# Optimization experiments

Hardware: AMD Instinct MI355X
Metric: run time of the kernel (lower is better)

Reference implementation:

```python
import jax, jax.numpy as jnp
import numpy as np

EPS = 1e-5

def _ln(x, g, b):
    mu = jnp.mean(x, axis=-1, keepdims=True)
    var = jnp.mean((x - mu) ** 2, axis=-1, keepdims=True)
    return (x - mu) * jax.lax.rsqrt(var + EPS) * g + b

def setup_inputs() -> dict:
    key = jax.random.key(0)
    B, V, I, H = 32, 48, 24, 768
    ks = jax.random.split(key, 10)
    s = 0.02
    return {
        'variables': jax.random.normal(ks[0], (B, V, H), jnp.float32),
        'interventions': jax.random.normal(ks[1], (B, I, H), jnp.float32),
        # variable_encoder: Linear(H,H) + LayerNorm(H)
        'W_enc': jax.random.normal(ks[2], (H, H), jnp.float32) * s,
        'b_enc': jnp.zeros((H,), jnp.float32),
        'g_enc': jnp.ones((H,), jnp.float32),
        'be_enc': jnp.zeros((H,), jnp.float32),
        # graph_generator: Linear(2H,H) + LN(H) + ReLU + Linear(H,1) + Sigmoid
        'Wg1': jax.random.normal(ks[3], (2 * H, H), jnp.float32) * s,
        'bg1': jnp.zeros((H,), jnp.float32),
        'g_g': jnp.ones((H,), jnp.float32),
        'b_g': jnp.zeros((H,), jnp.float32),
        'Wg2': jax.random.normal(ks[4], (H, 1), jnp.float32) * s,
        'bg2': jnp.zeros((1,), jnp.float32),
        # intervention_predictor: Linear(2H,H) + LN(H) + ReLU + Linear(H,H)
        'Wi1': jax.random.normal(ks[5], (2 * H, H), jnp.float32) * s,
        'bi1': jnp.zeros((H,), jnp.float32),
        'g_i': jnp.ones((H,), jnp.float32),
        'b_i': jnp.zeros((H,), jnp.float32),
        'Wi2': jax.random.normal(ks[6], (H, H), jnp.float32) * s,
        'bi2': jnp.zeros((H,), jnp.float32),
    }

def reference(variables, interventions, W_enc, b_enc, g_enc, be_enc,
              Wg1, bg1, g_g, b_g, Wg2, bg2, Wi1, bi1, g_i, b_i, Wi2, bi2):
    H = variables.shape[-1]
    V = variables.shape[1]
    # variable encoder: Linear + LayerNorm + ReLU
    enc = jax.nn.relu(_ln(variables @ W_enc + b_enc, g_enc, be_enc))  # [B,V,H]

    # graph generator over all ordered pairs (i,j): concat([enc_i, enc_j]) @ Wg1
    # split Wg1 so the concat-matmul becomes two small GEMMs + broadcast add
    hi = jnp.einsum('bvh,hk->bvk', enc, Wg1[:H])   # contribution of enc_i
    hj = jnp.einsum('bvh,hk->bvk', enc, Wg1[H:])   # contribution of enc_j
    h = jax.nn.relu(_ln(hi[:, :, None, :] + hj[:, None, :, :] + bg1, g_g, b_g))  # [B,V,V,H]
    score = jax.nn.sigmoid(jnp.squeeze(h @ Wg2, -1) + bg2[0])  # [B,V,V]
    # diagonal (i==j) is never written in the original -> stays zero
    causal_graph = score * (1.0 - jnp.eye(V, dtype=score.dtype))

    # intervention predictor: concat([intervention_i, enc_j]) -> MLP
    ha = jnp.einsum('bih,hk->bik', interventions, Wi1[:H])  # [B,I,H]
    hb = jnp.einsum('bvh,hk->bvk', enc, Wi1[H:])            # [B,V,H]
    h2 = jax.nn.relu(_ln(ha[:, :, None, :] + hb[:, None, :, :] + bi1, g_i, b_i))  # [B,I,V,H]
    effects = h2 @ Wi2 + bi2  # [B,I,V,H]

    return (effects, causal_graph, enc)
```

## Files before the change

kernel.cpp:

```cpp
#include <hip/hip_runtime.h>
#include <math.h>

#define Bp 32
#define Vp 48
#define Ip 24
#define Hp 768
#define EPS 1e-5f

#define EFFECTS_SIZE (Bp*Ip*Vp*Hp)
#define GRAPH_SIZE   (Bp*Vp*Vp)
#define ENC_SIZE     (Bp*Vp*Hp)
#define INT_SIZE     (Bp*Ip*Hp)
#define MS           (Hp*Hp)

typedef __attribute__((ext_vector_type(8))) short short8;
typedef __attribute__((ext_vector_type(4))) float floatx4;
typedef __attribute__((ext_vector_type(4))) unsigned int uintx4;

__device__ __forceinline__ unsigned short f2bf(float f) {
    unsigned int u = __float_as_uint(f);
    u += 0x7fffu + ((u >> 16) & 1u);
    return (unsigned short)(u >> 16);
}
__device__ __forceinline__ unsigned int f2bf2(float a, float b) {
    return (unsigned int)f2bf(a) | ((unsigned int)f2bf(b) << 16);
}

__global__ __launch_bounds__(256) void pack_weights(
    const float* __restrict__ W_enc, const float* __restrict__ Wg1,
    const float* __restrict__ Wi1, const float* __restrict__ Wi2,
    unsigned short* __restrict__ packed)
{
    const int bid = blockIdx.x;
    const int m = bid / 48;
    const int T = bid - m * 48;
    const float* src;
    switch (m) {
        case 0: src = W_enc; break;
        case 1: src = Wg1; break;
        case 2: src = Wg1 + Hp * Hp; break;
        case 3: src = Wi1 + Hp * Hp; break;
        case 4: src = Wi1; break;
        default: src = Wi2; break;
    }
    unsigned short* dst = packed + (size_t)m * MS;
    const int lane = threadIdx.x & 63;
    const int kq = threadIdx.x >> 6;
    const int col = T * 16 + (lane & 15);
    const int krow0 = (lane >> 4) * 8;
#pragma unroll
    for (int u = 0; u < 6; ++u) {
        const int kb = kq + 4 * u;
        unsigned int w[4];
#pragma unroll
        for (int p2 = 0; p2 < 4; ++p2) {
            float f0 = src[(size_t)(kb * 32 + krow0 + 2 * p2)     * Hp + col];
            float f1 = src[(size_t)(kb * 32 + krow0 + 2 * p2 + 1) * Hp + col];
            w[p2] = f2bf2(f0, f1);
        }
        uintx4 v; v.x = w[0]; v.y = w[1]; v.z = w[2]; v.w = w[3];
        *(uintx4*)(dst + ((size_t)(T * 24 + kb) * 64 + lane) * 8) = v;
    }
}

__global__ __launch_bounds__(256) void convert_inputs(
    const float* __restrict__ vars, const float* __restrict__ intv,
    const float* __restrict__ bg1, const float* __restrict__ bi1,
    unsigned short* __restrict__ varb, unsigned short* __restrict__ intvb,
    float* __restrict__ bias2304)
{
    const int p = blockIdx.x * 256 + threadIdx.x;
    const int VPn = ENC_SIZE / 2;
    if (p < VPn) {
        float2 f = ((const float2*)vars)[p];
        ((unsigned int*)varb)[p] = f2bf2(f.x, f.y);
    } else {
        int q = p - VPn;
        float2 f = ((const float2*)intv)[q];
        ((unsigned int*)intvb)[q] = f2bf2(f.x, f.y);
    }
    if (blockIdx.x == 0) {
        for (int t = threadIdx.x; t < 2304; t += 256)
            bias2304[t] = (t < 768) ? 0.0f : (t < 1536 ? bg1[t - 768] : bi1[t - 1536]);
    }
}

__global__ __launch_bounds__(256) void gemm_mfma(
    const unsigned short* __restrict__ A, const unsigned short* __restrict__ Bpk,
    const float* __restrict__ bias, float* __restrict__ C, int ldc)
{
    __shared__ unsigned short Asl[32 * 776];
    const int tid = threadIdx.x;
    const int wave = tid >> 6, lane = tid & 63;
    const int m0 = blockIdx.x * 32;
    const int n0 = blockIdx.y * 128;

#pragma unroll
    for (int u = 0; u < 12; ++u) {
        const int chunk = tid + 256 * u;
        const int r = chunk / 96, c = chunk - r * 96;
        uintx4 v = *(const uintx4*)(A + (size_t)(m0 + r) * Hp + c * 8);
        *(uintx4*)(&Asl[r * 776 + c * 8]) = v;
    }
    __syncthreads();

    const int mrow = lane & 15, kq = lane >> 4;
    const floatx4 z = {0.f, 0.f, 0.f, 0.f};
    floatx4 acc00 = z, acc01 = z, acc10 = z, acc11 = z;
    const int Tg0 = (n0 >> 4) + wave * 2;
    const unsigned short* Bb0 = Bpk + ((size_t)(Tg0 * 24) * 64 + lane) * 8;
    const unsigned short* Bb1 = Bpk + ((size_t)((Tg0 + 1) * 24) * 64 + lane) * 8;

#pragma unroll
    for (int kb = 0; kb < 24; ++kb) {
        short8 a0 = *(const short8*)&Asl[mrow * 776 + kb * 32 + kq * 8];
        short8 a1 = *(const short8*)&Asl[(16 + mrow) * 776 + kb * 32 + kq * 8];
        short8 b0 = *(const short8*)(Bb0 + (size_t)kb * 512);
        short8 b1 = *(const short8*)(Bb1 + (size_t)kb * 512);
        acc00 = __builtin_amdgcn_mfma_f32_16x16x32_bf16(a0, b0, acc00, 0, 0, 0);
        acc01 = __builtin_amdgcn_mfma_f32_16x16x32_bf16(a0, b1, acc01, 0, 0, 0);
        acc10 = __builtin_amdgcn_mfma_f32_16x16x32_bf16(a1, b0, acc10, 0, 0, 0);
        acc11 = __builtin_amdgcn_mfma_f32_16x16x32_bf16(a1, b1, acc11, 0, 0, 0);
    }

    floatx4 acc[2][2] = {{acc00, acc01}, {acc10, acc11}};
#pragma unroll
    for (int nt = 0; nt < 2; ++nt) {
        const int colg = n0 + wave * 32 + nt * 16 + mrow;
        const float bv = bias ? bias[colg] : 0.0f;
#pragma unroll
        for (int mt = 0; mt < 2; ++mt) {
#pragma unroll
            for (int r = 0; r < 4; ++r) {
                const int row = m0 + mt * 16 + kq * 4 + r;
                C[(size_t)row * ldc + colg] = acc[mt][nt][r] + bv;
            }
        }
    }
}

__global__ __launch_bounds__(256) void ln_relu(
    const float* __restrict__ pre, const float* __restrict__ g,
    const float* __restrict__ be, float* __restrict__ encf,
    unsigned short* __restrict__ encb)
{
    const int wave = threadIdx.x >> 6, lane = threadIdx.x & 63;
    const int row = blockIdx.x * 4 + wave;
    const float2* rp = (const float2*)(pre + (size_t)row * Hp);
    float2 x[6]; float s = 0.f, q = 0.f;
#pragma unroll
    for (int c = 0; c < 6; ++c) {
        x[c] = rp[lane + 64 * c];
        s += x[c].x + x[c].y;
        q += x[c].x * x[c].x + x[c].y * x[c].y;
    }
#pragma unroll
    for (int m = 1; m < 64; m <<= 1) { s += __shfl_xor(s, m, 64); q += __shfl_xor(q, m, 64); }
    const float mu = s * (1.0f / Hp);
    const float var = q * (1.0f / Hp) - mu * mu;
    const float rs = rsqrtf(var + EPS);
    float2* of = (float2*)(encf + (size_t)row * Hp);
    unsigned int* ob = (unsigned int*)(encb + (size_t)row * Hp);
#pragma unroll
    for (int c = 0; c < 6; ++c) {
        const float2 g2 = ((const float2*)g)[lane + 64 * c];
        const float2 b2 = ((const float2*)be)[lane + 64 * c];
        float y0 = fmaxf((x[c].x - mu) * rs * g2.x + b2.x, 0.f);
        float y1 = fmaxf((x[c].y - mu) * rs * g2.y + b2.y, 0.f);
        of[lane + 64 * c] = make_float2(y0, y1);
        ob[lane + 64 * c] = f2bf2(y0, y1);
    }
}

__global__ __launch_bounds__(256) void graph_kernel(
    const float* __restrict__ ws2, const float* __restrict__ gg_,
    const float* __restrict__ bb_, const float* __restrict__ Wg2,
    const float* __restrict__ bg2, float* __restrict__ out)
{
    const int wave = threadIdx.x >> 6, lane = threadIdx.x & 63;
    const int p = blockIdx.x;
    const int b = p / Vp, i = p - b * Vp;
    const float* hi_row = ws2 + (size_t)p * 2304;
    float ri[12], gg[12], bb[12], w2[12];
#pragma unroll
    for (int c = 0; c < 12; ++c) {
        const int k = lane + 64 * c;
        ri[c] = hi_row[k]; gg[c] = gg_[k]; bb[c] = bb_[k]; w2[c] = Wg2[k];
    }
    const float bg2v = bg2[0];
    const int j0 = wave * 12;
    for (int jj = 0; jj < 12; ++jj) {
        const int j = j0 + jj;
        const float* hj_row = ws2 + (size_t)(b * Vp + j) * 2304 + 768;
        float x[12], s = 0.f, q = 0.f;
#pragma unroll
        for (int c = 0; c < 12; ++c) {
            x[c] = ri[c] + hj_row[lane + 64 * c];
            s += x[c]; q += x[c] * x[c];
        }
#pragma unroll
        for (int m = 1; m < 64; m <<= 1) { s += __shfl_xor(s, m, 64); q += __shfl_xor(q, m, 64); }
        const float mu = s * (1.0f / Hp);
        const float var = q * (1.0f / Hp) - mu * mu;
        const float rs = rsqrtf(var + EPS);
        float pd = 0.f;
#pragma unroll
        for (int c = 0; c < 12; ++c) {
            float y = fmaxf((x[c] - mu) * rs * gg[c] + bb[c], 0.f);
            pd = fmaf(y, w2[c], pd);
        }
#pragma unroll
        for (int m = 1; m < 64; m <<= 1) pd += __shfl_xor(pd, m, 64);
        if (lane == 0) {
            float sc = (i == j) ? 0.0f : 1.0f / (1.0f + expf(-(pd + bg2v)));
            out[(size_t)p * Vp + j] = sc;
        }
    }
}

__global__ __launch_bounds__(256) void effects_mfma(
    const float* __restrict__ ha, const float* __restrict__ ws2,
    const float* __restrict__ g_i, const float* __restrict__ b_i,
    const unsigned short* __restrict__ Bpk, const float* __restrict__ bi2,
    float* __restrict__ out)
{
    __shared__ unsigned short Asl[32 * 776];
    const int tid = threadIdx.x, wave = tid >> 6, lane = tid & 63;
    const int m0 = blockIdx.x * 32;

    float2 gv[6], bv[6];
#pragma unroll
    for (int c = 0; c < 6; ++c) {
        gv[c] = ((const float2*)g_i)[lane + 64 * c];
        bv[c] = ((const float2*)b_i)[lane + 64 * c];
    }

#pragma unroll
    for (int u = 0; u < 8; ++u) {
        const int lr = wave * 8 + u;
        const int r = m0 + lr;
        const int bi = r / 48, j = r - bi * 48;
        const int b = bi / Ip;
        const float2* hap = (const float2*)(ha + (size_t)bi * Hp);
        const float2* hbp = (const float2*)(ws2 + (size_t)(b * Vp + j) * 2304 + 1536);
        float2 x[6]; float s = 0.f, q = 0.f;
#pragma unroll
        for (int c = 0; c < 6; ++c) {
            float2 a2 = hap[lane + 64 * c];
            float2 h2 = hbp[lane + 64 * c];
            x[c].x = a2.x + h2.x; x[c].y = a2.y + h2.y;
            s += x[c].x + x[c].y;
            q += x[c].x * x[c].x + x[c].y * x[c].y;
        }
#pragma unroll
        for (int m = 1; m < 64; m <<= 1) { s += __shfl_xor(s, m, 64); q += __shfl_xor(q, m, 64); }
        const float mu = s * (1.0f / Hp);
        const float var = q * (1.0f / Hp) - mu * mu;
        const float rs = rsqrtf(var + EPS);
#pragma unroll
        for (int c = 0; c < 6; ++c) {
            float y0 = fmaxf((x[c].x - mu) * rs * gv[c].x + bv[c].x, 0.f);
            float y1 = fmaxf((x[c].y - mu) * rs * gv[c].y + bv[c].y, 0.f);
            *(unsigned int*)(&Asl[lr * 776 + (lane + 64 * c) * 2]) = f2bf2(y0, y1);
        }
    }
    __syncthreads();

    const int mrow = lane & 15, kq = lane >> 4;
    const floatx4 z = {0.f, 0.f, 0.f, 0.f};
#pragma unroll
    for (int G = 0; G < 4; ++G) {
        const int Tg = wave * 12 + G * 3;
        floatx4 acc[2][3];
#pragma unroll
        for (int mt = 0; mt < 2; ++mt)
#pragma unroll
            for (int nt = 0; nt < 3; ++nt) acc[mt][nt] = z;
        const unsigned short* Bb0 = Bpk + ((size_t)((Tg + 0) * 24) * 64 + lane) * 8;
        const unsigned short* Bb1 = Bpk + ((size_t)((Tg + 1) * 24) * 64 + lane) * 8;
        const unsigned short* Bb2 = Bpk + ((size_t)((Tg + 2) * 24) * 64 + lane) * 8;
#pragma unroll
        for (int kb = 0; kb < 24; ++kb) {
            short8 a0 = *(const short8*)&Asl[mrow * 776 + kb * 32 + kq * 8];
            short8 a1 = *(const short8*)&Asl[(16 + mrow) * 776 + kb * 32 + kq * 8];
            short8 b0 = *(const short8*)(Bb0 + (size_t)kb * 512);
            short8 b1 = *(const short8*)(Bb1 + (size_t)kb * 512);
            short8 b2 = *(const short8*)(Bb2 + (size_t)kb * 512);
            acc[0][0] = __builtin_amdgcn_mfma_f32_16x16x32_bf16(a0, b0, acc[0][0], 0, 0, 0);
            acc[1][0] = __builtin_amdgcn_mfma_f32_16x16x32_bf16(a1, b0, acc[1][0], 0, 0, 0);
            acc[0][1] = __builtin_amdgcn_mfma_f32_16x16x32_bf16(a0, b1, acc[0][1], 0, 0, 0);
            acc[1][1] = __builtin_amdgcn_mfma_f32_16x16x32_bf16(a1, b1, acc[1][1], 0, 0, 0);
            acc[0][2] = __builtin_amdgcn_mfma_f32_16x16x32_bf16(a0, b2, acc[0][2], 0, 0, 0);
            acc[1][2] = __builtin_amdgcn_mfma_f32_16x16x32_bf16(a1, b2, acc[1][2], 0, 0, 0);
        }
#pragma unroll
        for (int nt = 0; nt < 3; ++nt) {
            const int colg = (Tg + nt) * 16 + mrow;
            const float biasv = bi2[colg];
#pragma unroll
            for (int mt = 0; mt < 2; ++mt) {
#pragma unroll
                for (int r = 0; r < 4; ++r) {
                    const int row = m0 + mt * 16 + kq * 4 + r;
                    out[(size_t)row * Hp + colg] = acc[mt][nt][r] + biasv;
                }
            }
        }
    }
}

extern "C" void kernel_launch(void* const* d_in, const int* in_sizes, int n_in,
                              void* d_out, int out_size, void* d_ws, size_t ws_size,
                              hipStream_t stream) {
    const float* variables     = (const float*)d_in[0];
    const float* interventions = (const float*)d_in[1];
    const float* W_enc  = (const float*)d_in[2];
    const float* b_enc  = (const float*)d_in[3];
    const float* g_enc  = (const float*)d_in[4];
    const float* be_enc = (const float*)d_in[5];
    const float* Wg1 = (const float*)d_in[6];
    const float* bg1 = (const float*)d_in[7];
    const float* g_g = (const float*)d_in[8];
    const float* b_g = (const float*)d_in[9];
    const float* Wg2 = (const float*)d_in[10];
    const float* bg2 = (const float*)d_in[11];
    const float* Wi1 = (const float*)d_in[12];
    const float* bi1 = (const float*)d_in[13];
    const float* g_i = (const float*)d_in[14];
    const float* b_i = (const float*)d_in[15];
    const float* Wi2 = (const float*)d_in[16];
    const float* bi2 = (const float*)d_in[17];

    float* out = (float*)d_out;
    float* effects = out;
    float* graph = out + EFFECTS_SIZE;
    float* enc_f = out + EFFECTS_SIZE + GRAPH_SIZE;

    char* wsb = (char*)d_ws;
    unsigned short* packedW = (unsigned short*)wsb;
    float* ws2  = (float*)(wsb + 7077888);
    float* pre1 = ws2;
    float* ha   = (float*)(wsb + 7077888 + 14155776);
    unsigned short* varb  = (unsigned short*)(wsb + 23592960);
    unsigned short* intvb = (unsigned short*)(wsb + 25952256);
    unsigned short* encb  = (unsigned short*)(wsb + 27131904);
    float* bias2304 = (float*)(wsb + 29491200);

    pack_weights<<<288, 256, 0, stream>>>(W_enc, Wg1, Wi1, Wi2, packedW);
    convert_inputs<<<3456, 256, 0, stream>>>(variables, interventions, bg1, bi1,
                                             varb, intvb, bias2304);
    gemm_mfma<<<dim3(48, 6), 256, 0, stream>>>(varb, packedW, b_enc, pre1, Hp);
    ln_relu<<<384, 256, 0, stream>>>(pre1, g_enc, be_enc, enc_f, encb);
    gemm_mfma<<<dim3(48, 18), 256, 0, stream>>>(encb, packedW + (size_t)1 * MS,
                                                bias2304, ws2, 2304);
    gemm_mfma<<<dim3(24, 6), 256, 0, stream>>>(intvb, packedW + (size_t)4 * MS,
                                               nullptr, ha, Hp);
    graph_kernel<<<Bp * Vp, 256, 0, stream>>>(ws2, g_g, b_g, Wg2, bg2, graph);
    effects_mfma<<<(Bp * Ip * Vp) / 32, 256, 0, stream>>>(ha, ws2, g_i, b_i,
                                                          packedW + (size_t)5 * MS,
                                                          bi2, effects);
}
```

Measured before the change: 329.7 us.

## Retile GEMMs to 48-row blocks with swizzled LDS and register prefetch

The GEMM and effects kernels now use 48-row blocks (one b,i pair per effects block), each wave computing a 3x6 grid of 16x16 MFMA tiles. A is stored in LDS in MFMA fragment order with an XOR swizzle, and B and A fragments are prefetched into rotating register buffers across k-steps. The aim is more operand reuse per load and better latency hiding, and the weight packing kernel is split into more blocks for parallelism. The costs are much higher register pressure and far fewer blocks for the small GEMMs (32 or 16), which could leave many CUs idle.

```diff
diff --git a/kernel.cpp b/kernel.cpp
--- a/kernel.cpp
+++ b/kernel.cpp
@@ -10,7 +10,6 @@
 #define EFFECTS_SIZE (Bp*Ip*Vp*Hp)
 #define GRAPH_SIZE   (Bp*Vp*Vp)
 #define ENC_SIZE     (Bp*Vp*Hp)
-#define INT_SIZE     (Bp*Ip*Hp)
 #define MS           (Hp*Hp)
 
 typedef __attribute__((ext_vector_type(8))) short short8;
@@ -32,8 +31,10 @@
     unsigned short* __restrict__ packed)
 {
     const int bid = blockIdx.x;
-    const int m = bid / 48;
-    const int T = bid - m * 48;
+    const int m = bid / 288;
+    const int rem = bid - m * 288;
+    const int T = rem / 6;
+    const int u = rem - T * 6;
     const float* src;
     switch (m) {
         case 0: src = W_enc; break;
@@ -48,19 +49,16 @@
     const int kq = threadIdx.x >> 6;
     const int col = T * 16 + (lane & 15);
     const int krow0 = (lane >> 4) * 8;
-#pragma unroll
-    for (int u = 0; u < 6; ++u) {
-        const int kb = kq + 4 * u;
-        unsigned int w[4];
-#pragma unroll
-        for (int p2 = 0; p2 < 4; ++p2) {
-            float f0 = src[(size_t)(kb * 32 + krow0 + 2 * p2)     * Hp + col];
-            float f1 = src[(size_t)(kb * 32 + krow0 + 2 * p2 + 1) * Hp + col];
-            w[p2] = f2bf2(f0, f1);
-        }
-        uintx4 v; v.x = w[0]; v.y = w[1]; v.z = w[2]; v.w = w[3];
-        *(uintx4*)(dst + ((size_t)(T * 24 + kb) * 64 + lane) * 8) = v;
-    }
+    const int kb = kq + 4 * u;
+    unsigned int w[4];
+#pragma unroll
+    for (int p2 = 0; p2 < 4; ++p2) {
+        float f0 = src[(size_t)(kb * 32 + krow0 + 2 * p2)     * Hp + col];
+        float f1 = src[(size_t)(kb * 32 + krow0 + 2 * p2 + 1) * Hp + col];
+        w[p2] = f2bf2(f0, f1);
+    }
+    uintx4 v; v.x = w[0]; v.y = w[1]; v.z = w[2]; v.w = w[3];
+    *(uintx4*)(dst + ((size_t)(T * 24 + kb) * 64 + lane) * 8) = v;
 }
 
 __global__ __launch_bounds__(256) void convert_inputs(
@@ -85,56 +83,82 @@
     }
 }
 
-__global__ __launch_bounds__(256) void gemm_mfma(
+__global__ __launch_bounds__(256) void gemm48(
     const unsigned short* __restrict__ A, const unsigned short* __restrict__ Bpk,
     const float* __restrict__ bias, float* __restrict__ C, int ldc)
 {
-    __shared__ unsigned short Asl[32 * 776];
-    const int tid = threadIdx.x;
-    const int wave = tid >> 6, lane = tid & 63;
-    const int m0 = blockIdx.x * 32;
-    const int n0 = blockIdx.y * 128;
-
-#pragma unroll
-    for (int u = 0; u < 12; ++u) {
-        const int chunk = tid + 256 * u;
-        const int r = chunk / 96, c = chunk - r * 96;
-        uintx4 v = *(const uintx4*)(A + (size_t)(m0 + r) * Hp + c * 8);
-        *(uintx4*)(&Asl[r * 776 + c * 8]) = v;
+    __shared__ unsigned short Asl[3 * 24 * 64 * 8];
+    const int tid = threadIdx.x, wave = tid >> 6, lane = tid & 63;
+    const int m0 = blockIdx.x * 48;
+
+#pragma unroll
+    for (int uu = 0; uu < 18; ++uu) {
+        const int s = tid + 256 * uu;
+        const int mt = s / 1536;
+        const int r2 = s - mt * 1536;
+        const int kb = r2 >> 6;
+        const int L  = r2 & 63;
+        const int mrow = L & 15, kq = L >> 4;
+        uintx4 v = *(const uintx4*)(A + (size_t)(m0 + mt * 16 + mrow) * Hp + kb * 32 + kq * 8);
+        const int phys = (mt * 24 + kb) * 64 + (L ^ (kb & 7));
+        *(uintx4*)(&Asl[phys * 8]) = v;
     }
     __syncthreads();
 
     const int mrow = lane & 15, kq = lane >> 4;
     const floatx4 z = {0.f, 0.f, 0.f, 0.f};
-    floatx4 acc00 = z, acc01 = z, acc10 = z, acc11 = z;
-    const int Tg0 = (n0 >> 4) + wave * 2;
-    const unsigned short* Bb0 = Bpk + ((size_t)(Tg0 * 24) * 64 + lane) * 8;
-    const unsigned short* Bb1 = Bpk + ((size_t)((Tg0 + 1) * 24) * 64 + lane) * 8;
-
-#pragma unroll
-    for (int kb = 0; kb < 24; ++kb) {
-        short8 a0 = *(const short8*)&Asl[mrow * 776 + kb * 32 + kq * 8];
-        short8 a1 = *(const short8*)&Asl[(16 + mrow) * 776 + kb * 32 + kq * 8];
-        short8 b0 = *(const short8*)(Bb0 + (size_t)kb * 512);
-        short8 b1 = *(const short8*)(Bb1 + (size_t)kb * 512);
-        acc00 = __builtin_amdgcn_mfma_f32_16x16x32_bf16(a0, b0, acc00, 0, 0, 0);
-        acc01 = __builtin_amdgcn_mfma_f32_16x16x32_bf16(a0, b1, acc01, 0, 0, 0);
-        acc10 = __builtin_amdgcn_mfma_f32_16x16x32_bf16(a1, b0, acc10, 0, 0, 0);
-        acc11 = __builtin_amdgcn_mfma_f32_16x16x32_bf16(a1, b1, acc11, 0, 0, 0);
-    }
-
-    floatx4 acc[2][2] = {{acc00, acc01}, {acc10, acc11}};
-#pragma unroll
-    for (int nt = 0; nt < 2; ++nt) {
-        const int colg = n0 + wave * 32 + nt * 16 + mrow;
-        const float bv = bias ? bias[colg] : 0.0f;
-#pragma unroll
-        for (int mt = 0; mt < 2; ++mt) {
-#pragma unroll
-            for (int r = 0; r < 4; ++r) {
-                const int row = m0 + mt * 16 + kq * 4 + r;
-                C[(size_t)row * ldc + colg] = acc[mt][nt][r] + bv;
+
+#pragma unroll
+    for (int G = 0; G < 2; ++G) {
+        const int Tg0 = blockIdx.y * 48 + wave * 12 + G * 6;
+        const unsigned short* Bbase = Bpk + (size_t)Tg0 * 12288 + lane * 8;
+        floatx4 acc[3][6];
+#pragma unroll
+        for (int mt = 0; mt < 3; ++mt)
+#pragma unroll
+            for (int nt = 0; nt < 6; ++nt) acc[mt][nt] = z;
+
+        short8 bbuf[3][6], abuf[2][3];
+#pragma unroll
+        for (int nt = 0; nt < 6; ++nt) {
+            bbuf[0][nt] = *(const short8*)(Bbase + (size_t)nt * 12288);
+            bbuf[1][nt] = *(const short8*)(Bbase + (size_t)nt * 12288 + 512);
+        }
+#pragma unroll
+        for (int mt = 0; mt < 3; ++mt)
+            abuf[0][mt] = *(const short8*)(&Asl[((mt * 24) * 64 + lane) * 8]);
+
+#pragma unroll
+        for (int kb = 0; kb < 24; ++kb) {
+            if (kb + 2 < 24) {
+#pragma unroll
+                for (int nt = 0; nt < 6; ++nt)
+                    bbuf[(kb + 2) % 3][nt] =
+                        *(const short8*)(Bbase + (size_t)nt * 12288 + (kb + 2) * 512);
             }
+            if (kb + 1 < 24) {
+#pragma unroll
+                for (int mt = 0; mt < 3; ++mt)
+                    abuf[(kb + 1) & 1][mt] = *(const short8*)(
+                        &Asl[((mt * 24 + kb + 1) * 64 + (lane ^ ((kb + 1) & 7))) * 8]);
+            }
+#pragma unroll
+            for (int mt = 0; mt < 3; ++mt)
+#pragma unroll
+                for (int nt = 0; nt < 6; ++nt)
+                    acc[mt][nt] = __builtin_amdgcn_mfma_f32_16x16x32_bf16(
+                        abuf[kb & 1][mt], bbuf[kb % 3][nt], acc[mt][nt], 0, 0, 0);
+        }
+
+#pragma unroll
+        for (int nt = 0; nt < 6; ++nt) {
+            const int colg = (Tg0 + nt) * 16 + mrow;
+            const float bv = bias ? bias[colg] : 0.0f;
+#pragma unroll
+            for (int mt = 0; mt < 3; ++mt)
+#pragma unroll
+                for (int r = 0; r < 4; ++r)
+                    C[(size_t)(m0 + mt * 16 + kq * 4 + r) * ldc + colg] = acc[mt][nt][r] + bv;
         }
     }
 }
@@ -218,50 +242,67 @@
     }
 }
 
-__global__ __launch_bounds__(256) void effects_mfma(
+__global__ __launch_bounds__(256) void effects48(
     const float* __restrict__ ha, const float* __restrict__ ws2,
     const float* __restrict__ g_i, const float* __restrict__ b_i,
     const unsigned short* __restrict__ Bpk, const float* __restrict__ bi2,
     float* __restrict__ out)
 {
-    __shared__ unsigned short Asl[32 * 776];
+    __shared__ unsigned short Asl[3 * 24 * 64 * 8];
     const int tid = threadIdx.x, wave = tid >> 6, lane = tid & 63;
-    const int m0 = blockIdx.x * 32;
-
-    float2 gv[6], bv[6];
-#pragma unroll
-    for (int c = 0; c < 6; ++c) {
-        gv[c] = ((const float2*)g_i)[lane + 64 * c];
-        bv[c] = ((const float2*)b_i)[lane + 64 * c];
-    }
-
-#pragma unroll
-    for (int u = 0; u < 8; ++u) {
-        const int lr = wave * 8 + u;
-        const int r = m0 + lr;
-        const int bi = r / 48, j = r - bi * 48;
-        const int b = bi / Ip;
-        const float2* hap = (const float2*)(ha + (size_t)bi * Hp);
-        const float2* hbp = (const float2*)(ws2 + (size_t)(b * Vp + j) * 2304 + 1536);
-        float2 x[6]; float s = 0.f, q = 0.f;
+    const int bi = blockIdx.x;
+    const int b = bi / Ip;
+    const int half = lane >> 5, hl = lane & 31;
+
+    const floatx4* hap = (const floatx4*)(ha + (size_t)bi * Hp);
+    const floatx4* gp = (const floatx4*)g_i;
+    const floatx4* bp = (const floatx4*)b_i;
+    floatx4 hav[6], gv[6], bv[6];
+#pragma unroll
+    for (int t = 0; t < 3; ++t) {
+        hav[2*t]   = hap[2*hl + 64*t];     hav[2*t+1] = hap[2*hl + 1 + 64*t];
+        gv[2*t]    = gp[2*hl + 64*t];      gv[2*t+1]  = gp[2*hl + 1 + 64*t];
+        bv[2*t]    = bp[2*hl + 64*t];      bv[2*t+1]  = bp[2*hl + 1 + 64*t];
+    }
+
+#pragma unroll
+    for (int p = 0; p < 6; ++p) {
+        const int u = wave * 12 + 2 * p + half;
+        const floatx4* hbp = (const floatx4*)(ws2 + (size_t)(b * Vp + u) * 2304 + 1536);
+        floatx4 x[6]; float s = 0.f, q = 0.f;
+#pragma unroll
+        for (int t = 0; t < 3; ++t) {
+            x[2*t]   = hav[2*t]   + hbp[2*hl + 64*t];
+            x[2*t+1] = hav[2*t+1] + hbp[2*hl + 1 + 64*t];
+        }
 #pragma unroll
         for (int c = 0; c < 6; ++c) {
-            float2 a2 = hap[lane + 64 * c];
-            float2 h2 = hbp[lane + 64 * c];
-            x[c].x = a2.x + h2.x; x[c].y = a2.y + h2.y;
-            s += x[c].x + x[c].y;
-            q += x[c].x * x[c].x + x[c].y * x[c].y;
-        }
-#pragma unroll
-        for (int m = 1; m < 64; m <<= 1) { s += __shfl_xor(s, m, 64); q += __shfl_xor(q, m, 64); }
+            s += x[c].x + x[c].y + x[c].z + x[c].w;
+            q += x[c].x*x[c].x + x[c].y*x[c].y + x[c].z*x[c].z + x[c].w*x[c].w;
+        }
+#pragma unroll
+        for (int m = 1; m < 32; m <<= 1) { s += __shfl_xor(s, m, 64); q += __shfl_xor(q, m, 64); }
         const float mu = s * (1.0f / Hp);
         const float var = q * (1.0f / Hp) - mu * mu;
         const float rs = rsqrtf(var + EPS);
-#pragma unroll
-        for (int c = 0; c < 6; ++c) {
-            float y0 = fmaxf((x[c].x - mu) * rs * gv[c].x + bv[c].x, 0.f);
-            float y1 = fmaxf((x[c].y - mu) * rs * gv[c].y + bv[c].y, 0.f);
-            *(unsigned int*)(&Asl[lr * 776 + (lane + 64 * c) * 2]) = f2bf2(y0, y1);
+        const int mt = u >> 4, mrow = u & 15;
+#pragma unroll
+        for (int t = 0; t < 3; ++t) {
+            float y0 = fmaxf((x[2*t].x   - mu) * rs * gv[2*t].x   + bv[2*t].x,   0.f);
+            float y1 = fmaxf((x[2*t].y   - mu) * rs * gv[2*t].y   + bv[2*t].y,   0.f);
+            float y2 = fmaxf((x[2*t].z   - mu) * rs * gv[2*t].z   + bv[2*t].z,   0.f);
+            float y3 = fmaxf((x[2*t].w   - mu) * rs * gv[2*t].w   + bv[2*t].w,   0.f);
+            float y4 = fmaxf((x[2*t+1].x - mu) * rs * gv[2*t+1].x + bv[2*t+1].x, 0.f);
+            float y5 = fmaxf((x[2*t+1].y - mu) * rs * gv[2*t+1].y + bv[2*t+1].y, 0.f);
+            float y6 = fmaxf((x[2*t+1].z - mu) * rs * gv[2*t+1].z + bv[2*t+1].z, 0.f);
+            float y7 = fmaxf((x[2*t+1].w - mu) * rs * gv[2*t+1].w + bv[2*t+1].w, 0.f);
+            const int cpk = hl + 32 * t;
+            const int kb = cpk >> 2, kq2 = cpk & 3;
+            const int phys = (mt * 24 + kb) * 64 + ((kq2 * 16 + mrow) ^ (kb & 7));
+            uintx4 v;
+            v.x = f2bf2(y0, y1); v.y = f2bf2(y2, y3);
+            v.z = f2bf2(y4, y5); v.w = f2bf2(y6, y7);
+            *(uintx4*)(&Asl[phys * 8]) = v;
         }
     }
     __syncthreads();
@@ -269,40 +310,57 @@
     const int mrow = lane & 15, kq = lane >> 4;
     const floatx4 z = {0.f, 0.f, 0.f, 0.f};
 #pragma unroll
-    for (int G = 0; G < 4; ++G) {
-        const int Tg = wave * 12 + G * 3;
-        floatx4 acc[2][3];
-#pragma unroll
-        for (int mt = 0; mt < 2; ++mt)
-#pragma unroll
-            for (int nt = 0; nt < 3; ++nt) acc[mt][nt] = z;
-        const unsigned short* Bb0 = Bpk + ((size_t)((Tg + 0) * 24) * 64 + lane) * 8;
-        const unsigned short* Bb1 = Bpk + ((size_t)((Tg + 1) * 24) * 64 + lane) * 8;
-        const unsigned short* Bb2 = Bpk + ((size_t)((Tg + 2) * 24) * 64 + lane) * 8;
+    for (int G = 0; G < 2; ++G) {
+        const int Tg0 = wave * 12 + G * 6;
+        const unsigned short* Bbase = Bpk + (size_t)Tg0 * 12288 + lane * 8;
+        floatx4 acc[3][6];
+#pragma unroll
+        for (int mt = 0; mt < 3; ++mt)
+#pragma unroll
+            for (int nt = 0; nt < 6; ++nt) acc[mt][nt] = z;
+
+        short8 bbuf[3][6], abuf[2][3];
+#pragma unroll
+        for (int nt = 0; nt < 6; ++nt) {
+            bbuf[0][nt] = *(const short8*)(Bbase + (size_t)nt * 12288);
+            bbuf[1][nt] = *(const short8*)(Bbase + (size_t)nt * 12288 + 512);
+        }
+#pragma unroll
+        for (int mt = 0; mt < 3; ++mt)
+            abuf[0][mt] = *(const short8*)(&Asl[((mt * 24) * 64 + lane) * 8]);
+
 #pragma unroll
         for (int kb = 0; kb < 24; ++kb) {
-            short8 a0 = *(const short8*)&Asl[mrow * 776 + kb * 32 + kq * 8];
-            short8 a1 = *(const short8*)&Asl[(16 + mrow) * 776 + kb * 32 + kq * 8];
-            short8 b0 = *(const short8*)(Bb0 + (size_t)kb * 512);
-            short8 b1 = *(const short8*)(Bb1 + (size_t)kb * 512);
-            short8 b2 = *(const short8*)(Bb2 + (size_t)kb * 512);
-            acc[0][0] = __builtin_amdgcn_mfma_f32_16x16x32_bf16(a0, b0, acc[0][0], 0, 0, 0);
-            acc[1][0] = __builtin_amdgcn_mfma_f32_16x16x32_bf16(a1, b0, acc[1][0], 0, 0, 0);
-            acc[0][1] = __builtin_amdgcn_mfma_f32_16x16x32_bf16(a0, b1, acc[0][1], 0, 0, 0);
-            acc[1][1] = __builtin_amdgcn_mfma_f32_16x16x32_bf16(a1, b1, acc[1][1], 0, 0, 0);
-            acc[0][2] = __builtin_amdgcn_mfma_f32_16x16x32_bf16(a0, b2, acc[0][2], 0, 0, 0);
-            acc[1][2] = __builtin_amdgcn_mfma_f32_16x16x32_bf16(a1, b2, acc[1][2], 0, 0, 0);
-        }
-#pragma unroll
-        for (int nt = 0; nt < 3; ++nt) {
-            const int colg = (Tg + nt) * 16 + mrow;
+            if (kb + 2 < 24) {
+#pragma unroll
+                for (int nt = 0; nt < 6; ++nt)
+                    bbuf[(kb + 2) % 3][nt] =
+                        *(const short8*)(Bbase + (size_t)nt * 12288 + (kb + 2) * 512);
+            }
+            if (kb + 1 < 24) {
+#pragma unroll
+                for (int mt = 0; mt < 3; ++mt)
+                    abuf[(kb + 1) & 1][mt] = *(const short8*)(
+                        &Asl[((mt * 24 + kb + 1) * 64 + (lane ^ ((kb + 1) & 7))) * 8]);
+            }
+#pragma unroll
+            for (int mt = 0; mt < 3; ++mt)
+#pragma unroll
+                for (int nt = 0; nt < 6; ++nt)
+                    acc[mt][nt] = __builtin_amdgcn_mfma_f32_16x16x32_bf16(
+                        abuf[kb & 1][mt], bbuf[kb % 3][nt], acc[mt][nt], 0, 0, 0);
+        }
+
+#pragma unroll
+        for (int nt = 0; nt < 6; ++nt) {
+            const int colg = (Tg0 + nt) * 16 + mrow;
             const float biasv = bi2[colg];
 #pragma unroll
-            for (int mt = 0; mt < 2; ++mt) {
+            for (int mt = 0; mt < 3; ++mt) {
 #pragma unroll
                 for (int r = 0; r < 4; ++r) {
-                    const int row = m0 + mt * 16 + kq * 4 + r;
-                    out[(size_t)row * Hp + colg] = acc[mt][nt][r] + biasv;
+                    out[(size_t)(bi * 48 + mt * 16 + kq * 4 + r) * Hp + colg] =
+                        acc[mt][nt][r] + biasv;
                 }
             }
         }
@@ -346,17 +404,16 @@
     unsigned short* encb  = (unsigned short*)(wsb + 27131904);
     float* bias2304 = (float*)(wsb + 29491200);
 
-    pack_weights<<<288, 256, 0, stream>>>(W_enc, Wg1, Wi1, Wi2, packedW);
+    pack_weights<<<1728, 256, 0, stream>>>(W_enc, Wg1, Wi1, Wi2, packedW);
     convert_inputs<<<3456, 256, 0, stream>>>(variables, interventions, bg1, bi1,
                                              varb, intvb, bias2304);
-    gemm_mfma<<<dim3(48, 6), 256, 0, stream>>>(varb, packedW, b_enc, pre1, Hp);
+    gemm48<<<dim3(32, 1), 256, 0, stream>>>(varb, packedW, b_enc, pre1, Hp);
     ln_relu<<<384, 256, 0, stream>>>(pre1, g_enc, be_enc, enc_f, encb);
-    gemm_mfma<<<dim3(48, 18), 256, 0, stream>>>(encb, packedW + (size_t)1 * MS,
-                                                bias2304, ws2, 2304);
-    gemm_mfma<<<dim3(24, 6), 256, 0, stream>>>(intvb, packedW + (size_t)4 * MS,
-                                               nullptr, ha, Hp);
+    gemm48<<<dim3(32, 3), 256, 0, stream>>>(encb, packedW + (size_t)1 * MS,
+                                            bias2304, ws2, 2304);
+    gemm48<<<dim3(16, 1), 256, 0, stream>>>(intvb, packedW + (size_t)4 * MS,
+                                            nullptr, ha, Hp);
     graph_kernel<<<Bp * Vp, 256, 0, stream>>>(ws2, g_g, b_g, Wg2, bg2, graph);
-    effects_mfma<<<(Bp * Ip * Vp) / 32, 256, 0, stream>>>(ha, ws2, g_i, b_i,
-                                                          packedW + (size_t)5 * MS,
-                                                          bi2, effects);
-}
+    effects48<<<Bp * Ip, 256, 0, stream>>>(ha, ws2, g_i, b_i,
+                                           packedW + (size_t)5 * MS, bi2, effects);
+}
```

After: 335.8 us. About the same (+1.9%).
